# Kernel optimization log

Hardware: AMD Instinct MI355X
Metric: run time of the kernel (lower is better)

The kernel has to match this reference:

```python
import jax, jax.numpy as jnp
import numpy as np

NUM_HEADS = 12
NUM_BLOCKS = 12
EPS = 1e-5


def _layernorm(x, g, b):
    mu = jnp.mean(x, axis=-1, keepdims=True)
    var = jnp.mean(jnp.square(x - mu), axis=-1, keepdims=True)
    return (x - mu) * jax.lax.rsqrt(var + EPS) * g + b


def setup_inputs() -> dict:
    key = jax.random.key(0)
    ks = jax.random.split(key, 16)
    B, N, D, F = 4, 512, 768, 3072
    s = 1.0 / np.sqrt(D)
    sf = 1.0 / np.sqrt(F)
    return {
        "x": jax.random.normal(ks[0], (B, N, D), jnp.float32),
        "Wq": jax.random.normal(ks[1], (D, D), jnp.float32) * s,
        "bq": jnp.zeros((D,), jnp.float32),
        "Wk": jax.random.normal(ks[2], (D, D), jnp.float32) * s,
        "bk": jnp.zeros((D,), jnp.float32),
        "Wv": jax.random.normal(ks[3], (D, D), jnp.float32) * s,
        "bv": jnp.zeros((D,), jnp.float32),
        "g1": jnp.ones((D,), jnp.float32),
        "be1": jnp.zeros((D,), jnp.float32),
        "g2": jnp.ones((D,), jnp.float32),
        "be2": jnp.zeros((D,), jnp.float32),
        "W0": jax.random.normal(ks[4], (D, F), jnp.float32) * s,
        "b0": jnp.zeros((F,), jnp.float32),
        "W1": jax.random.normal(ks[5], (F, D), jnp.float32) * sf,
        "b1": jnp.zeros((D,), jnp.float32),
    }


def _attention(x, Wq, bq, Wk, bk, Wv, bv):
    B, N, D = x.shape
    H = NUM_HEADS
    hd = D // H
    q = (x @ Wq + bq).reshape(B, N, H, hd)
    k = (x @ Wk + bk).reshape(B, N, H, hd)
    v = (x @ Wv + bv).reshape(B, N, H, hd)
    # scores: [B, H, N, N], scaled by 1/sqrt(head_dim)
    scores = jnp.einsum("bqhd,bkhd->bhqk", q, k) / np.sqrt(hd)
    weights = jax.nn.softmax(scores, axis=-1)
    out = jnp.einsum("bhqk,bkhd->bqhd", weights, v)
    return out.reshape(B, N, D)


def reference(x, Wq, bq, Wk, bk, Wv, bv, g1, be1, g2, be2, W0, b0, W1, b1):
    # All blocks share the same weights (module appends the same block instance).
    for _ in range(NUM_BLOCKS):
        x = x + _attention(_layernorm(x, g1, be1), Wq, bq, Wk, bk, Wv, bv)
        h = _layernorm(x, g2, be2)
        h = jax.nn.gelu(h @ W0 + b0, approximate=False) @ W1 + b1
        x = x + h
    return x
```

## Files before the change

kernel.cpp:

```cpp
#include <hip/hip_runtime.h>
#include <stdint.h>

typedef float  f32x4  __attribute__((ext_vector_type(4)));
typedef __bf16 bf16x8 __attribute__((ext_vector_type(8)));
typedef short  s16x8  __attribute__((ext_vector_type(8)));

#define DEV __device__ __forceinline__

DEV short f2b(float f) {
    union { float f; unsigned u; } c; c.f = f;
    unsigned u = c.u;
    unsigned r = (u + 0x7fffu + ((u >> 16) & 1u)) >> 16;
    return (short)r;
}
DEV float b2f(short s) {
    union { unsigned u; float f; } c; c.u = ((unsigned)(unsigned short)s) << 16;
    return c.f;
}

DEV void gload_lds16(const void* g, void* l) {
    __builtin_amdgcn_global_load_lds(
        (const __attribute__((address_space(1))) void*)g,
        (__attribute__((address_space(3))) void*)l, 16, 0, 0);
}

template<int BM, int BN, int MODE, int NSPLIT>
__global__ __launch_bounds__(256) void gemm_bt(
    const short* __restrict__ A, const short* __restrict__ Bt,
    const float* __restrict__ bias,
    float* __restrict__ outf, short* __restrict__ outs0,
    short* __restrict__ outs1, short* __restrict__ outs2,
    long sA, long sB, long sO, int M, int N, int K)
{
    constexpr int BK = 64;
    constexpr int FM = BM / 32, FN = BN / 32;
    __shared__ __align__(16) short As[2][BM * BK];
    __shared__ __align__(16) short Bs[2][BN * BK];

    const int tid  = threadIdx.x;
    const int w    = tid >> 6, lane = tid & 63;
    const int wr   = w >> 1,  wc   = w & 1;
    const int l16  = lane & 15, lhi = lane >> 4, sw = lane & 7;

    const int gx   = gridDim.x;
    const int nwg  = gx * gridDim.y;
    const int flat = blockIdx.y * gx + blockIdx.x;
    const int nf   = (flat & 7) * (nwg >> 3) + (flat >> 3);
    const int bx   = nf % gx, by = nf / gx;

    int z, kz;
    if constexpr (NSPLIT > 1) { z = 0; kz = blockIdx.z; }
    else                      { z = blockIdx.z; kz = 0; }

    const short* Ab = A  + (long)z * sA + (long)by * BM * K;
    const short* Bb = Bt + (long)z * sB + (long)bx * BN * K;

    const int ktPer = (K >> 6) / NSPLIT;
    const int ktBeg = kz * ktPer, ktEnd = ktBeg + ktPer;

    f32x4 acc[FM][FN];
#pragma unroll
    for (int m = 0; m < FM; ++m)
#pragma unroll
        for (int n = 0; n < FN; ++n) acc[m][n] = (f32x4)(0.0f);

    auto stage = [&](int buf, int kt) {
        const short* Ag = Ab + kt * BK;
#pragma unroll
        for (int i = 0; i < BM / 32; ++i) {
            int seg = i * 256 + tid;
            int row = seg >> 3;
            int gcs = (tid & 7) ^ (row & 7);
            gload_lds16(Ag + (long)row * K + gcs * 8, &As[buf][(i * 256 + w * 64) * 8]);
        }
        const short* Bg = Bb + kt * BK;
#pragma unroll
        for (int i = 0; i < BN / 32; ++i) {
            int seg = i * 256 + tid;
            int row = seg >> 3;
            int gcs = (tid & 7) ^ (row & 7);
            gload_lds16(Bg + (long)row * K + gcs * 8, &Bs[buf][(i * 256 + w * 64) * 8]);
        }
    };

    stage(0, ktBeg);
    asm volatile("s_waitcnt vmcnt(0)" ::: "memory");
    __builtin_amdgcn_s_barrier();

    int cur = 0;
    for (int kt = ktBeg; kt < ktEnd; ++kt) {
        if (kt + 1 < ktEnd) stage(cur ^ 1, kt + 1);
        const short* Ac = &As[cur][0];
        const short* Bc = &Bs[cur][0];
#pragma unroll
        for (int kk = 0; kk < 2; ++kk) {
            bf16x8 af[FM], bfr[FN];
#pragma unroll
            for (int m = 0; m < FM; ++m) {
                int ar = wr * (BM / 2) + m * 16 + l16;
                int ks = (kk * 4 + lhi) ^ sw;
                af[m] = *(const bf16x8*)(Ac + ar * BK + ks * 8);
            }
#pragma unroll
            for (int n = 0; n < FN; ++n) {
                int br = wc * (BN / 2) + n * 16 + l16;
                int ks = (kk * 4 + lhi) ^ sw;
                bfr[n] = *(const bf16x8*)(Bc + br * BK + ks * 8);
            }
#pragma unroll
            for (int m = 0; m < FM; ++m)
#pragma unroll
                for (int n = 0; n < FN; ++n)
                    acc[m][n] = __builtin_amdgcn_mfma_f32_16x16x32_bf16(
                        af[m], bfr[n], acc[m][n], 0, 0, 0);
        }
        asm volatile("s_waitcnt vmcnt(0)" ::: "memory");
        __builtin_amdgcn_s_barrier();
        cur ^= 1;
    }

    const int m0 = by * BM, n0 = bx * BN;
#pragma unroll
    for (int m = 0; m < FM; ++m) {
#pragma unroll
        for (int n = 0; n < FN; ++n) {
            const int grow0 = m0 + wr * (BM / 2) + m * 16 + lhi * 4;
            const int gcol  = n0 + wc * (BN / 2) + n * 16 + l16;
#pragma unroll
            for (int r = 0; r < 4; ++r) {
                float val = acc[m][n][r];
                int grow = grow0 + r;
                if constexpr (MODE == 1) {
                    float v = val + bias[gcol];
                    int d  = gcol & 63;
                    int hh = gcol >> 6;
                    int bb = grow >> 9, s = grow & 511;
                    if (hh < 12) {
                        outs0[((long)((bb * 12 + hh) * 512 + s) << 6) + d] = f2b(v * 0.125f);
                    } else if (hh < 24) {
                        outs1[((long)((bb * 12 + (hh - 12)) * 512 + s) << 6) + d] = f2b(v);
                    } else {
                        outs2[((long)((bb * 12 + (hh - 24)) * 64 + d) << 9) + s] = f2b(v);
                    }
                } else if constexpr (MODE == 2) {
                    float v = val + bias[gcol];
                    v = 0.5f * v * (1.0f + erff(v * 0.70710678118f));
                    outs0[(long)grow * N + gcol] = f2b(v);
                } else {
                    outf[(long)kz * M * N + (long)grow * N + gcol] = val;
                }
            }
        }
    }
}

__global__ __launch_bounds__(256) void ffn2_reduce(
    const float* __restrict__ part, const float* __restrict__ bias,
    float* __restrict__ x)
{
    int i4 = blockIdx.x * 256 + threadIdx.x;
    const float4* p0 = (const float4*)part;
    const float4* p1 = (const float4*)(part + 2048l * 768);
    const float4* b4 = (const float4*)bias;
    float4* x4 = (float4*)x;
    float4 a = p0[i4], b = p1[i4], bb = b4[i4 % 192], xv = x4[i4];
    xv.x += a.x + b.x + bb.x;
    xv.y += a.y + b.y + bb.y;
    xv.z += a.z + b.z + bb.z;
    xv.w += a.w + b.w + bb.w;
    x4[i4] = xv;
}

__global__ __launch_bounds__(256) void attn_fused(
    const short* __restrict__ Qg,
    const short* __restrict__ Kg,
    const short* __restrict__ VTg,
    float* __restrict__ x)
{
    __shared__ __align__(16) short Qs[64 * 64];
    __shared__ __align__(16) short Ks[2][64 * 64];
    __shared__ __align__(16) short Vs[2][64 * 64];
    __shared__ __align__(16) short Ps[4][16 * 64];

    const int tid = threadIdx.x;
    const int w = tid >> 6, lane = tid & 63;
    const int l16 = lane & 15, lhi = lane >> 4;

    const int f  = blockIdx.y * 8 + blockIdx.x;
    const int nf = (f & 7) * 48 + (f >> 3);
    const int z  = nf >> 3, qt = nf & 7;
    const int q0 = qt * 64;

    const short* Qb = Qg  + (long)z * 512 * 64 + q0 * 64;
    const short* Kb = Kg  + (long)z * 512 * 64;
    const short* Vb = VTg + (long)z * 64 * 512;

    auto stageQ = [&]() {
#pragma unroll
        for (int i = 0; i < 2; ++i) {
            int seg = i * 256 + tid;
            int row = seg >> 3;
            int gc  = (seg & 7) ^ (row & 7);
            gload_lds16(Qb + row * 64 + gc * 8, Qs + (i * 256 + w * 64) * 8);
        }
    };
    auto stageK = [&](int buf, int kt) {
#pragma unroll
        for (int i = 0; i < 2; ++i) {
            int seg = i * 256 + tid;
            int row = seg >> 3;
            int gc  = (seg & 7) ^ (row & 7);
            gload_lds16(Kb + (kt * 64 + row) * 64 + gc * 8, &Ks[buf][(i * 256 + w * 64) * 8]);
        }
    };
    auto stageV = [&](int buf, int kt) {
#pragma unroll
        for (int i = 0; i < 2; ++i) {
            int seg = i * 256 + tid;
            int row = seg >> 3;
            int gc  = (seg & 7) ^ (row & 7);
            gload_lds16(Vb + (long)row * 512 + kt * 64 + gc * 8, &Vs[buf][(i * 256 + w * 64) * 8]);
        }
    };

    stageQ(); stageK(0, 0); stageV(0, 0);
    asm volatile("s_waitcnt vmcnt(0)" ::: "memory");
    __syncthreads();

    bf16x8 bq[2];
    {
        int qr = w * 16 + l16;
#pragma unroll
        for (int kk = 0; kk < 2; ++kk)
            bq[kk] = *(const bf16x8*)(Qs + qr * 64 + (((kk * 4 + lhi) ^ (l16 & 7)) * 8));
    }

    float m = -3e38f, l = 0.0f;
    f32x4 acc[4];
#pragma unroll
    for (int bn = 0; bn < 4; ++bn) acc[bn] = (f32x4)(0.0f);

    int cur = 0;
    for (int kt = 0; kt < 8; ++kt) {
        if (kt < 7) { stageK(cur ^ 1, kt + 1); stageV(cur ^ 1, kt + 1); }

        f32x4 s[4];
#pragma unroll
        for (int km = 0; km < 4; ++km) s[km] = (f32x4)(0.0f);
#pragma unroll
        for (int kk = 0; kk < 2; ++kk) {
#pragma unroll
            for (int km = 0; km < 4; ++km) {
                int kr = km * 16 + l16;
                bf16x8 ak = *(const bf16x8*)(&Ks[cur][kr * 64 + (((kk * 4 + lhi) ^ (l16 & 7)) * 8)]);
                s[km] = __builtin_amdgcn_mfma_f32_16x16x32_bf16(ak, bq[kk], s[km], 0, 0, 0);
            }
        }

        float tmax = -3e38f;
#pragma unroll
        for (int km = 0; km < 4; ++km)
#pragma unroll
            for (int r = 0; r < 4; ++r) tmax = fmaxf(tmax, s[km][r]);
        tmax = fmaxf(tmax, __shfl_xor(tmax, 16));
        tmax = fmaxf(tmax, __shfl_xor(tmax, 32));
        float mn = fmaxf(m, tmax);
        float sc = __expf(m - mn);
        float p[16];
        float ts = 0.0f;
#pragma unroll
        for (int km = 0; km < 4; ++km)
#pragma unroll
            for (int r = 0; r < 4; ++r) {
                float e = __expf(s[km][r] - mn);
                p[km * 4 + r] = e; ts += e;
            }
        ts += __shfl_xor(ts, 16);
        ts += __shfl_xor(ts, 32);
        l = l * sc + ts; m = mn;

        float scr[4];
#pragma unroll
        for (int r = 0; r < 4; ++r) scr[r] = __shfl(sc, lhi * 4 + r);
#pragma unroll
        for (int bn = 0; bn < 4; ++bn)
#pragma unroll
            for (int r = 0; r < 4; ++r) acc[bn][r] *= scr[r];

        {
            short* Pw = &Ps[w][0];
#pragma unroll
            for (int km = 0; km < 4; ++km)
#pragma unroll
                for (int r = 0; r < 4; ++r) {
                    int k = km * 16 + lhi * 4 + r;
                    int g = k >> 3, e = k & 7;
                    Pw[l16 * 64 + ((g ^ (l16 & 7)) * 8) + e] = f2b(p[km * 4 + r]);
                }
        }

#pragma unroll
        for (int kk = 0; kk < 2; ++kk) {
            bf16x8 ap = *(const bf16x8*)(&Ps[w][l16 * 64 + (((kk * 4 + lhi) ^ (l16 & 7)) * 8)]);
#pragma unroll
            for (int bn = 0; bn < 4; ++bn) {
                int vr = bn * 16 + l16;
                bf16x8 bv = *(const bf16x8*)(&Vs[cur][vr * 64 + (((kk * 4 + lhi) ^ (l16 & 7)) * 8)]);
                acc[bn] = __builtin_amdgcn_mfma_f32_16x16x32_bf16(ap, bv, acc[bn], 0, 0, 0);
            }
        }

        asm volatile("s_waitcnt vmcnt(0)" ::: "memory");
        __builtin_amdgcn_s_barrier();
        cur ^= 1;
    }

    float inv = 1.0f / l;
    float invr[4];
#pragma unroll
    for (int r = 0; r < 4; ++r) invr[r] = __shfl(inv, lhi * 4 + r);
    const int zb = z / 12, zh = z - (z / 12) * 12;
#pragma unroll
    for (int bn = 0; bn < 4; ++bn)
#pragma unroll
        for (int r = 0; r < 4; ++r) {
            long idx = ((long)(zb * 512 + q0 + w * 16 + lhi * 4 + r)) * 768 + zh * 64 + bn * 16 + l16;
            x[idx] += acc[bn][r] * invr[r];
        }
}

__global__ __launch_bounds__(256) void ln_kernel(
    const float* __restrict__ x, const float* __restrict__ g,
    const float* __restrict__ be, short* __restrict__ out)
{
    int row  = blockIdx.x * 4 + (threadIdx.x >> 6);
    int lane = threadIdx.x & 63;
    const float4* xr = (const float4*)(x + (long)row * 768);
    float4 v0 = xr[lane], v1 = xr[lane + 64], v2 = xr[lane + 128];
    float f[12] = {v0.x, v0.y, v0.z, v0.w, v1.x, v1.y, v1.z, v1.w, v2.x, v2.y, v2.z, v2.w};

    float s = 0.f;
#pragma unroll
    for (int j = 0; j < 12; ++j) s += f[j];
#pragma unroll
    for (int o = 32; o; o >>= 1) s += __shfl_xor(s, o);
    float mu = s * (1.0f / 768.0f);
    float s2 = 0.f;
#pragma unroll
    for (int j = 0; j < 12; ++j) { f[j] -= mu; s2 += f[j] * f[j]; }
#pragma unroll
    for (int o = 32; o; o >>= 1) s2 += __shfl_xor(s2, o);
    float rstd = rsqrtf(s2 * (1.0f / 768.0f) + 1e-5f);

    const float4* gr = (const float4*)g;
    const float4* br = (const float4*)be;
    short4* orow = (short4*)(out + (long)row * 768);
#pragma unroll
    for (int jb = 0; jb < 3; ++jb) {
        float4 gg = gr[lane + 64 * jb], bb = br[lane + 64 * jb];
        short4 o4;
        o4.x = f2b(f[4 * jb + 0] * rstd * gg.x + bb.x);
        o4.y = f2b(f[4 * jb + 1] * rstd * gg.y + bb.y);
        o4.z = f2b(f[4 * jb + 2] * rstd * gg.z + bb.z);
        o4.w = f2b(f[4 * jb + 3] * rstd * gg.w + bb.w);
        orow[lane + 64 * jb] = o4;
    }
}

__global__ __launch_bounds__(256) void transpose_w(
    const float* __restrict__ in, short* __restrict__ out, int R, int C)
{
    __shared__ float t[32][33];
    int r0 = blockIdx.y * 32, c0 = blockIdx.x * 32;
    int tx = threadIdx.x & 31, ty = threadIdx.x >> 5;
#pragma unroll
    for (int p = 0; p < 4; ++p)
        t[ty + 8 * p][tx] = in[(long)(r0 + ty + 8 * p) * C + c0 + tx];
    __syncthreads();
#pragma unroll
    for (int p = 0; p < 4; ++p)
        out[(long)(c0 + ty + 8 * p) * R + r0 + tx] = f2b(t[tx][ty + 8 * p]);
}

__global__ void concat_bias(const float* __restrict__ bq, const float* __restrict__ bk,
                            const float* __restrict__ bv, float* __restrict__ o)
{
    int i = blockIdx.x * 256 + threadIdx.x;
    if (i < 768) { o[i] = bq[i]; o[768 + i] = bk[i]; o[1536 + i] = bv[i]; }
}

extern "C" void kernel_launch(void* const* d_in, const int* in_sizes, int n_in,
                              void* d_out, int out_size, void* d_ws, size_t ws_size,
                              hipStream_t stream)
{
    (void)in_sizes; (void)n_in; (void)out_size; (void)ws_size;
    const float* x_in = (const float*)d_in[0];
    const float* Wq  = (const float*)d_in[1];
    const float* bq  = (const float*)d_in[2];
    const float* Wk  = (const float*)d_in[3];
    const float* bk  = (const float*)d_in[4];
    const float* Wv  = (const float*)d_in[5];
    const float* bv  = (const float*)d_in[6];
    const float* g1  = (const float*)d_in[7];
    const float* be1 = (const float*)d_in[8];
    const float* g2  = (const float*)d_in[9];
    const float* be2 = (const float*)d_in[10];
    const float* W0  = (const float*)d_in[11];
    const float* b0  = (const float*)d_in[12];
    const float* W1  = (const float*)d_in[13];
    const float* b1  = (const float*)d_in[14];

    float* x = (float*)d_out;

    char* ws = (char*)d_ws;
    size_t off = 0;
    auto alloc = [&](size_t bytes) -> char* {
        char* p = ws + off; off = (off + bytes + 255) & ~(size_t)255; return p;
    };
    short* wqkvt = (short*)alloc(2304l * 768 * 2);
    short* w0t   = (short*)alloc(3072l * 768 * 2);
    short* w1t   = (short*)alloc(768l * 3072 * 2);
    float* bqkv  = (float*)alloc(2304 * 4);
    short* lnb   = (short*)alloc(2048l * 768 * 2);
    short* q     = (short*)alloc(2048l * 768 * 2);
    short* k     = (short*)alloc(2048l * 768 * 2);
    short* vt    = (short*)alloc(2048l * 768 * 2);
    short* h     = (short*)alloc(2048l * 3072 * 2);
    float* part  = (float*)alloc(2l * 2048 * 768 * 4);

    hipMemcpyAsync(x, x_in, 2048l * 768 * 4, hipMemcpyDeviceToDevice, stream);

    transpose_w<<<dim3(24, 24), 256, 0, stream>>>(Wq, wqkvt, 768, 768);
    transpose_w<<<dim3(24, 24), 256, 0, stream>>>(Wk, wqkvt + 768l * 768, 768, 768);
    transpose_w<<<dim3(24, 24), 256, 0, stream>>>(Wv, wqkvt + 2l * 768 * 768, 768, 768);
    transpose_w<<<dim3(96, 24), 256, 0, stream>>>(W0, w0t, 768, 3072);
    transpose_w<<<dim3(24, 96), 256, 0, stream>>>(W1, w1t, 3072, 768);
    concat_bias<<<3, 256, 0, stream>>>(bq, bk, bv, bqkv);

    for (int it = 0; it < 12; ++it) {
        ln_kernel<<<512, 256, 0, stream>>>(x, g1, be1, lnb);
        gemm_bt<64, 64, 1, 1><<<dim3(36, 32, 1), 256, 0, stream>>>(
            lnb, wqkvt, bqkv, nullptr, q, k, vt, 0, 0, 0, 2048, 2304, 768);
        attn_fused<<<dim3(8, 48), 256, 0, stream>>>(q, k, vt, x);
        ln_kernel<<<512, 256, 0, stream>>>(x, g2, be2, lnb);
        gemm_bt<64, 64, 2, 1><<<dim3(48, 32, 1), 256, 0, stream>>>(
            lnb, w0t, b0, nullptr, h, nullptr, nullptr, 0, 0, 0, 2048, 3072, 768);
        gemm_bt<64, 64, 3, 2><<<dim3(12, 32, 2), 256, 0, stream>>>(
            h, w1t, nullptr, part, nullptr, nullptr, nullptr, 0, 0, 0, 2048, 768, 3072);
        ffn2_reduce<<<1536, 256, 0, stream>>>(part, b1, x);
    }
}
```

Before: 1.160 ms.

## Triple-buffer GEMM K-loop and fuse FFN2 reduction with next LayerNorm

The GEMM mainloop moves from double to triple buffering of LDS tiles. It prefetches two stages ahead and waits with vmcnt(4), so one stage of global loads can stay in flight during the MFMA work. The split-K reduction kernel becomes row-wise and also computes the next block's first LayerNorm, which removes one ln_kernel launch and one re-read of x per iteration. The costs are 1.5x LDS per GEMM block, which may reduce occupancy, and a vmcnt scheme that relies on exactly 4 loads per stage.

Measured after the change: 1.165 ms. Within noise of the previous version (+0.4%).

```diff
diff --git a/kernel.cpp b/kernel.cpp
--- a/kernel.cpp
+++ b/kernel.cpp
@@ -34,8 +34,9 @@
 {
     constexpr int BK = 64;
     constexpr int FM = BM / 32, FN = BN / 32;
-    __shared__ __align__(16) short As[2][BM * BK];
-    __shared__ __align__(16) short Bs[2][BN * BK];
+    static_assert((BM + BN) / 32 == 4, "vmcnt(4) assumes 4 loads per stage");
+    __shared__ __align__(16) short As[3][BM * BK];
+    __shared__ __align__(16) short Bs[3][BN * BK];
 
     const int tid  = threadIdx.x;
     const int w    = tid >> 6, lane = tid & 63;
@@ -84,12 +85,15 @@
     };
 
     stage(0, ktBeg);
-    asm volatile("s_waitcnt vmcnt(0)" ::: "memory");
+    stage(1, ktBeg + 1);
+    asm volatile("s_waitcnt vmcnt(4)" ::: "memory");
     __builtin_amdgcn_s_barrier();
 
     int cur = 0;
     for (int kt = ktBeg; kt < ktEnd; ++kt) {
-        if (kt + 1 < ktEnd) stage(cur ^ 1, kt + 1);
+        const bool more = (kt + 2 < ktEnd);
+        if (more) stage(cur >= 1 ? cur - 1 : cur + 2, kt + 2);
+
         const short* Ac = &As[cur][0];
         const short* Bc = &Bs[cur][0];
 #pragma unroll
@@ -114,9 +118,10 @@
                     acc[m][n] = __builtin_amdgcn_mfma_f32_16x16x32_bf16(
                         af[m], bfr[n], acc[m][n], 0, 0, 0);
         }
-        asm volatile("s_waitcnt vmcnt(0)" ::: "memory");
+        if (more) asm volatile("s_waitcnt vmcnt(4)" ::: "memory");
+        else      asm volatile("s_waitcnt vmcnt(0)" ::: "memory");
         __builtin_amdgcn_s_barrier();
-        cur ^= 1;
+        cur = (cur + 1 == 3) ? 0 : cur + 1;
     }
 
     const int m0 = by * BM, n0 = bx * BN;
@@ -154,21 +159,61 @@
     }
 }
 
-__global__ __launch_bounds__(256) void ffn2_reduce(
+template<int DO_LN>
+__global__ __launch_bounds__(256) void ffn2_reduce_ln(
     const float* __restrict__ part, const float* __restrict__ bias,
-    float* __restrict__ x)
-{
-    int i4 = blockIdx.x * 256 + threadIdx.x;
-    const float4* p0 = (const float4*)part;
-    const float4* p1 = (const float4*)(part + 2048l * 768);
+    float* __restrict__ x, const float* __restrict__ g,
+    const float* __restrict__ be, short* __restrict__ out)
+{
+    int row  = blockIdx.x * 4 + (threadIdx.x >> 6);
+    int lane = threadIdx.x & 63;
+    const float4* p0 = (const float4*)part + (long)row * 192;
+    const float4* p1 = (const float4*)(part + 2048l * 768) + (long)row * 192;
     const float4* b4 = (const float4*)bias;
-    float4* x4 = (float4*)x;
-    float4 a = p0[i4], b = p1[i4], bb = b4[i4 % 192], xv = x4[i4];
-    xv.x += a.x + b.x + bb.x;
-    xv.y += a.y + b.y + bb.y;
-    xv.z += a.z + b.z + bb.z;
-    xv.w += a.w + b.w + bb.w;
-    x4[i4] = xv;
+    float4* xr = (float4*)(x + (long)row * 768);
+
+    float f[12];
+#pragma unroll
+    for (int jb = 0; jb < 3; ++jb) {
+        int idx = lane + 64 * jb;
+        float4 a = p0[idx], b = p1[idx], c = b4[idx], xv = xr[idx];
+        xv.x += a.x + b.x + c.x;
+        xv.y += a.y + b.y + c.y;
+        xv.z += a.z + b.z + c.z;
+        xv.w += a.w + b.w + c.w;
+        xr[idx] = xv;
+        f[4 * jb + 0] = xv.x; f[4 * jb + 1] = xv.y;
+        f[4 * jb + 2] = xv.z; f[4 * jb + 3] = xv.w;
+    }
+
+    if constexpr (DO_LN) {
+        float s = 0.f;
+#pragma unroll
+        for (int j = 0; j < 12; ++j) s += f[j];
+#pragma unroll
+        for (int o = 32; o; o >>= 1) s += __shfl_xor(s, o);
+        float mu = s * (1.0f / 768.0f);
+        float s2 = 0.f;
+#pragma unroll
+        for (int j = 0; j < 12; ++j) { f[j] -= mu; s2 += f[j] * f[j]; }
+#pragma unroll
+        for (int o = 32; o; o >>= 1) s2 += __shfl_xor(s2, o);
+        float rstd = rsqrtf(s2 * (1.0f / 768.0f) + 1e-5f);
+
+        const float4* gr = (const float4*)g;
+        const float4* br = (const float4*)be;
+        short4* orow = (short4*)(out + (long)row * 768);
+#pragma unroll
+        for (int jb = 0; jb < 3; ++jb) {
+            float4 gg = gr[lane + 64 * jb], bb = br[lane + 64 * jb];
+            short4 o4;
+            o4.x = f2b(f[4 * jb + 0] * rstd * gg.x + bb.x);
+            o4.y = f2b(f[4 * jb + 1] * rstd * gg.y + bb.y);
+            o4.z = f2b(f[4 * jb + 2] * rstd * gg.z + bb.z);
+            o4.w = f2b(f[4 * jb + 3] * rstd * gg.w + bb.w);
+            orow[lane + 64 * jb] = o4;
+        }
+    }
 }
 
 __global__ __launch_bounds__(256) void attn_fused(
@@ -438,7 +483,8 @@
     concat_bias<<<3, 256, 0, stream>>>(bq, bk, bv, bqkv);
 
     for (int it = 0; it < 12; ++it) {
-        ln_kernel<<<512, 256, 0, stream>>>(x, g1, be1, lnb);
+        if (it == 0)
+            ln_kernel<<<512, 256, 0, stream>>>(x, g1, be1, lnb);
         gemm_bt<64, 64, 1, 1><<<dim3(36, 32, 1), 256, 0, stream>>>(
             lnb, wqkvt, bqkv, nullptr, q, k, vt, 0, 0, 0, 2048, 2304, 768);
         attn_fused<<<dim3(8, 48), 256, 0, stream>>>(q, k, vt, x);
@@ -447,6 +493,9 @@
             lnb, w0t, b0, nullptr, h, nullptr, nullptr, 0, 0, 0, 2048, 3072, 768);
         gemm_bt<64, 64, 3, 2><<<dim3(12, 32, 2), 256, 0, stream>>>(
             h, w1t, nullptr, part, nullptr, nullptr, nullptr, 0, 0, 0, 2048, 768, 3072);
-        ffn2_reduce<<<1536, 256, 0, stream>>>(part, b1, x);
-    }
-}
+        if (it < 11)
+            ffn2_reduce_ln<1><<<512, 256, 0, stream>>>(part, b1, x, g1, be1, lnb);
+        else
+            ffn2_reduce_ln<0><<<512, 256, 0, stream>>>(part, b1, x, nullptr, nullptr, nullptr);
+    }
+}
```
